# Kernel tuning notes

Measured on AMD Instinct MI355X. Metric: run time of the kernel, lower is better.

Reference implementation:

```python
import jax, jax.numpy as jnp
import numpy as np

HEADS = 4
DIM_HEAD = 32


def setup_inputs() -> dict:
    key = jax.random.key(0)
    k1, k2, k3, k4 = jax.random.split(key, 4)
    dim = 256
    hidden = HEADS * DIM_HEAD  # 128
    x = jax.random.normal(k1, (4, dim, 64, 64), dtype=jnp.float32)
    # 1x1 convs are channel-mixing matmuls; store weights as [out_ch, in_ch]
    w_qkv = jax.random.normal(k2, (3 * hidden, dim), dtype=jnp.float32) * (dim ** -0.5)
    w_out = jax.random.normal(k3, (dim, hidden), dtype=jnp.float32) * (hidden ** -0.5)
    b_out = jax.random.normal(k4, (dim,), dtype=jnp.float32) * 0.02
    return {"x": x, "w_qkv": w_qkv, "w_out": w_out, "b_out": b_out}


def reference(x, w_qkv, w_out, b_out):
    b, c, h, w = x.shape
    n = h * w
    scale = DIM_HEAD ** -0.5
    xf = x.reshape(b, c, n)                                   # b c n
    qkv = jnp.einsum('oc,bcn->bon', w_qkv, xf)                # b (3*H*D) n
    q, k, v = jnp.split(qkv, 3, axis=1)                       # each b (H*D) n
    q = q.reshape(b, HEADS, DIM_HEAD, n) * scale              # b h d n
    k = k.reshape(b, HEADS, DIM_HEAD, n)
    v = v.reshape(b, HEADS, DIM_HEAD, n)
    sim = jnp.einsum('bhdi,bhdj->bhij', q, k)                 # b h n n
    attn = jax.nn.softmax(sim, axis=-1)                       # stable max-subtract inside
    out = jnp.einsum('bhij,bhdj->bhdi', attn, v)              # b h d n
    out = out.reshape(b, HEADS * DIM_HEAD, n)                 # b (h d) n
    out = jnp.einsum('oc,bcn->bon', w_out, out) + b_out[None, :, None]
    return out.reshape(b, -1, h, w)
```

## Files before the change

### kernel.cpp

```cpp
#include <hip/hip_runtime.h>
#include <hip/hip_bf16.h>
#include <stdint.h>

#define B_SZ 4
#define C_IN 256
#define N_SP 4096
#define HEADS 4
#define DH 32
#define HID 128

#define BI 128
#define BJ 64
#define JHALF 2048
#define PP 68

typedef short short4v __attribute__((ext_vector_type(4)));
typedef short short8 __attribute__((ext_vector_type(8)));
typedef float f32x4 __attribute__((ext_vector_type(4)));

#if __has_builtin(__builtin_amdgcn_exp2f)
#define EXP2 __builtin_amdgcn_exp2f
#else
#define EXP2 exp2f
#endif

__device__ __forceinline__ short f2bfs(float f) {
  return (short)((__float_as_uint(f) + 0x8000u) >> 16);
}
__device__ __forceinline__ float bfs2f(short s) {
  return __uint_as_float(((uint32_t)(unsigned short)s) << 16);
}
__device__ __forceinline__ short8 ld_frag(const short* p) {
  short4v a = *(const short4v*)p;
  short4v b = *(const short4v*)(p + 4);
  return __builtin_shufflevector(a, b, 0, 1, 2, 3, 4, 5, 6, 7);
}
__device__ __forceinline__ f32x4 mfma16(short8 a, short8 b, f32x4 c) {
  return __builtin_amdgcn_mfma_f32_16x16x32_bf16(a, b, c, 0, 0, 0);
}

__global__ __launch_bounds__(256) void prep_k(
    const float* __restrict__ x, const float* __restrict__ w_qkv,
    const float* __restrict__ w_out,
    short* __restrict__ xh, short* __restrict__ xl,
    short* __restrict__ wqh, short* __restrict__ wql,
    short* __restrict__ woh, short* __restrict__ wol) {
  const int t = threadIdx.x;
  const int bx = blockIdx.x;
  if (bx < 1024) {
    __shared__ float T[64 * 65];
    const int b = bx >> 8, n0 = ((bx >> 2) & 63) * 64, c0 = (bx & 3) * 64;
    const float* xb = x + (size_t)b * C_IN * N_SP;
    {
      const int n = t & 63, cw = t >> 6;
#pragma unroll
      for (int i = 0; i < 16; ++i) {
        const int c = cw * 16 + i;
        T[n * 65 + c] = xb[(size_t)(c0 + c) * N_SP + n0 + n];
      }
    }
    __syncthreads();
    {
      const int n = t >> 2, cg = t & 3;
#pragma unroll
      for (int j = 0; j < 2; ++j) {
        const int c = cg * 16 + j * 8;
        short8 hv, lv;
#pragma unroll
        for (int e = 0; e < 8; ++e) {
          const float v = T[n * 65 + c + e];
          const short hh = f2bfs(v);
          hv[e] = hh;
          lv[e] = f2bfs(v - bfs2f(hh));
        }
        const size_t off = ((size_t)(b * N_SP + n0 + n)) * C_IN + c0 + c;
        *(short8*)(xh + off) = hv;
        *(short8*)(xl + off) = lv;
      }
    }
  } else {
    const int f0 = (bx - 1024) * 8192;
#pragma unroll
    for (int j = 0; j < 32; ++j) {
      const int f = f0 + j * 256 + t;
      float v;
      short *dh, *dl;
      int idx;
      if (f < 384 * 256) { v = w_qkv[f]; dh = wqh; dl = wql; idx = f; }
      else { idx = f - 384 * 256; v = w_out[idx]; dh = woh; dl = wol; }
      const short hh = f2bfs(v);
      dh[idx] = hh;
      dl[idx] = f2bfs(v - bfs2f(hh));
    }
  }
}

__global__ __launch_bounds__(256) void qkv_mfma_k(
    const short* __restrict__ xh, const short* __restrict__ xl,
    const short* __restrict__ wqh, const short* __restrict__ wql,
    short* __restrict__ qt, short* __restrict__ kt, short* __restrict__ vt) {
  const int t = threadIdx.x;
  const int lane = t & 63, w = t >> 6;
  const int l15 = lane & 15, quad = lane >> 4;
  const int osec = blockIdx.y, b = blockIdx.z;
  const int n0 = blockIdx.x * 64 + w * 16;
  const size_t xrow = ((size_t)(b * N_SP + n0 + l15)) * C_IN;
  const size_t wrow = ((size_t)(osec * 128 + l15)) * C_IN;
  const bool isv = (osec == 2);
  const f32x4 zz = {0.f, 0.f, 0.f, 0.f};
  f32x4 acc[8];
#pragma unroll
  for (int ot = 0; ot < 8; ++ot) acc[ot] = zz;

  for (int k0 = 0; k0 < C_IN; k0 += 32) {
    const int ko = k0 + quad * 8;
    const short8 xhf = *(const short8*)(xh + xrow + ko);
    const short8 xlf = *(const short8*)(xl + xrow + ko);
#pragma unroll
    for (int ot = 0; ot < 8; ++ot) {
      const size_t wo = wrow + (size_t)ot * 16 * C_IN + ko;
      const short8 whf = *(const short8*)(wqh + wo);
      const short8 wlf = *(const short8*)(wql + wo);
      if (isv) {
        acc[ot] = mfma16(xhf, whf, acc[ot]);
        acc[ot] = mfma16(xlf, whf, acc[ot]);
        acc[ot] = mfma16(xhf, wlf, acc[ot]);
      } else {
        acc[ot] = mfma16(whf, xhf, acc[ot]);
        acc[ot] = mfma16(whf, xlf, acc[ot]);
        acc[ot] = mfma16(wlf, xhf, acc[ot]);
      }
    }
  }

  if (!isv) {
    const float sc = osec ? 1.f : (0.17677669529663687f * 1.4426950408889634f);
    short* dst = osec ? kt : qt;
    const int n = n0 + l15;
#pragma unroll
    for (int ot = 0; ot < 8; ++ot) {
      const int ol = ot * 16 + quad * 4;
      const int h = ol >> 5, d0 = ol & 31;
      short4v p;
#pragma unroll
      for (int r = 0; r < 4; ++r) p[r] = f2bfs(acc[ot][r] * sc);
      *(short4v*)(dst + ((size_t)(b * HEADS + h) * N_SP + n) * DH + d0) = p;
    }
  } else {
    const int n = n0 + quad * 4;
#pragma unroll
    for (int ot = 0; ot < 8; ++ot) {
      const int ol = ot * 16 + l15;
      const int h = ol >> 5, d = ol & 31;
      short4v p;
#pragma unroll
      for (int r = 0; r < 4; ++r) p[r] = f2bfs(acc[ot][r]);
      *(short4v*)(vt + ((size_t)(b * HEADS + h) * DH + d) * N_SP + n) = p;
    }
  }
}

__global__ __launch_bounds__(256, 2) void attn_k(
    const short* __restrict__ qt, const short* __restrict__ kt,
    const short* __restrict__ vt, float* __restrict__ po,
    float* __restrict__ lws) {
  __shared__ short Ps[BI * PP];
  __shared__ float Osh[DH * 132];
  const int t = threadIdx.x;
  const int lane = t & 63, w = t >> 6;
  const int l15 = lane & 15, quad = lane >> 4;
  const int i0 = blockIdx.x * BI;
  const int bh = blockIdx.y;
  const int part = blockIdx.z;
  const int jbase = part * JHALF;
  const short* qg = qt + ((size_t)bh * N_SP + i0) * DH;
  const short* kg = kt + ((size_t)bh * N_SP + jbase) * DH;
  const short* vg = vt + (size_t)bh * DH * N_SP + jbase;

  short8 bq[2];
#pragma unroll
  for (int tt = 0; tt < 2; ++tt)
    bq[tt] = *(const short8*)(qg + (size_t)(w * 32 + tt * 16 + l15) * DH + quad * 8);

  const f32x4 zz = {0.f, 0.f, 0.f, 0.f};
  f32x4 o_acc[2][2] = {{zz, zz}, {zz, zz}};
  float lsum[2] = {0.f, 0.f};
  short* prow[2];
#pragma unroll
  for (int tt = 0; tt < 2; ++tt) prow[tt] = Ps + (w * 32 + tt * 16 + l15) * PP;

  short8 akA[4], akB[4], vbA[2][2], vbB[2][2];
#pragma unroll
  for (int jt = 0; jt < 4; ++jt)
    akA[jt] = *(const short8*)(kg + (size_t)(jt * 16 + l15) * DH + quad * 8);
#pragma unroll
  for (int dt = 0; dt < 2; ++dt)
#pragma unroll
    for (int kk = 0; kk < 2; ++kk)
      vbA[dt][kk] = *(const short8*)(vg + (size_t)(dt * 16 + l15) * N_SP + kk * 32 + quad * 8);

  auto body = [&](const short8 (&akc)[4], const short8 (&vbc)[2][2],
                  short8 (&akn)[4], short8 (&vbn)[2][2], int jn) {
    f32x4 sf[2][4];
    __builtin_amdgcn_s_setprio(1);
#pragma unroll
    for (int tt = 0; tt < 2; ++tt)
#pragma unroll
      for (int jt = 0; jt < 4; ++jt) sf[tt][jt] = mfma16(akc[jt], bq[tt], zz);
    __builtin_amdgcn_s_setprio(0);
#pragma unroll
    for (int jt = 0; jt < 4; ++jt)
      akn[jt] = *(const short8*)(kg + (size_t)(jn + jt * 16 + l15) * DH + quad * 8);
#pragma unroll
    for (int dt = 0; dt < 2; ++dt)
#pragma unroll
      for (int kk = 0; kk < 2; ++kk)
        vbn[dt][kk] = *(const short8*)(vg + (size_t)(dt * 16 + l15) * N_SP + jn + kk * 32 + quad * 8);
#pragma unroll
    for (int tt = 0; tt < 2; ++tt)
#pragma unroll
      for (int jt = 0; jt < 4; ++jt) {
        const float e0 = EXP2(sf[tt][jt][0]);
        const float e1 = EXP2(sf[tt][jt][1]);
        const float e2 = EXP2(sf[tt][jt][2]);
        const float e3 = EXP2(sf[tt][jt][3]);
        lsum[tt] += (e0 + e1) + (e2 + e3);
        uint2 pk;
        asm("v_cvt_pk_bf16_f32 %0, %1, %2" : "=v"(pk.x) : "v"(e0), "v"(e1));
        asm("v_cvt_pk_bf16_f32 %0, %1, %2" : "=v"(pk.y) : "v"(e2), "v"(e3));
        *(uint2*)(prow[tt] + jt * 16 + quad * 4) = pk;
      }
    asm volatile("s_waitcnt lgkmcnt(0)" ::: "memory");
    short8 pa[2][2];
#pragma unroll
    for (int tt = 0; tt < 2; ++tt)
#pragma unroll
      for (int kk = 0; kk < 2; ++kk) pa[tt][kk] = ld_frag(prow[tt] + kk * 32 + quad * 8);
    __builtin_amdgcn_s_setprio(1);
#pragma unroll
    for (int tt = 0; tt < 2; ++tt)
#pragma unroll
      for (int dt = 0; dt < 2; ++dt) {
        o_acc[tt][dt] = mfma16(pa[tt][0], vbc[dt][0], o_acc[tt][dt]);
        o_acc[tt][dt] = mfma16(pa[tt][1], vbc[dt][1], o_acc[tt][dt]);
      }
    __builtin_amdgcn_s_setprio(0);
  };

  for (int jo = 0; jo < JHALF; jo += 2 * BJ) {
    body(akA, vbA, akB, vbB, (jo + BJ) & (JHALF - 1));
    body(akB, vbB, akA, vbA, (jo + 2 * BJ) & (JHALF - 1));
  }

#pragma unroll
  for (int tt = 0; tt < 2; ++tt) {
    lsum[tt] += __shfl_xor(lsum[tt], 16);
    lsum[tt] += __shfl_xor(lsum[tt], 32);
  }
  if (lane < 16) {
#pragma unroll
    for (int tt = 0; tt < 2; ++tt)
      lws[((size_t)(part * 16 + bh)) * N_SP + i0 + w * 32 + tt * 16 + lane] = lsum[tt];
  }
#pragma unroll
  for (int tt = 0; tt < 2; ++tt)
#pragma unroll
    for (int dt = 0; dt < 2; ++dt)
#pragma unroll
      for (int r = 0; r < 4; ++r)
        Osh[(dt * 16 + l15) * 132 + w * 32 + tt * 16 + quad * 4 + r] = o_acc[tt][dt][r];
  __syncthreads();
  {
    const int ii = t & 127, half = t >> 7;
    const int b = bh >> 2, h = bh & 3;
    float* dst = po + ((size_t)((part * B_SZ + b) * N_SP) + i0 + ii) * HID +
                 h * 32 + half * 16;
#pragma unroll
    for (int j4 = 0; j4 < 4; ++j4) {
      float4 vv;
      vv.x = Osh[(half * 16 + j4 * 4 + 0) * 132 + ii];
      vv.y = Osh[(half * 16 + j4 * 4 + 1) * 132 + ii];
      vv.z = Osh[(half * 16 + j4 * 4 + 2) * 132 + ii];
      vv.w = Osh[(half * 16 + j4 * 4 + 3) * 132 + ii];
      *(float4*)(dst + j4 * 4) = vv;
    }
  }
}

__global__ __launch_bounds__(256) void out_mfma_k(
    const float* __restrict__ po, const float* __restrict__ lws,
    const short* __restrict__ woh, const short* __restrict__ wol,
    const float* __restrict__ bias, float* __restrict__ out) {
  const int t = threadIdx.x;
  const int lane = t & 63, w = t >> 6;
  const int l15 = lane & 15, quad = lane >> 4;
  const int osec = blockIdx.y, b = blockIdx.z;
  const int n0 = blockIdx.x * 64 + w * 16;
  const int n = n0 + l15;
  const size_t PSTR = (size_t)B_SZ * N_SP * HID;
  const float* arow = po + ((size_t)(b * N_SP) + n) * HID;
  const size_t wrow = ((size_t)(osec * 128 + l15)) * HID;
  const f32x4 zz = {0.f, 0.f, 0.f, 0.f};
  f32x4 acc[8];
#pragma unroll
  for (int ot = 0; ot < 8; ++ot) acc[ot] = zz;

  for (int k0 = 0; k0 < HID; k0 += 32) {
    const int ko = k0 + quad * 8;
    const int h = k0 >> 5;
    const int bh = b * HEADS + h;
    const float lv = lws[(size_t)bh * N_SP + n] + lws[(size_t)(16 + bh) * N_SP + n];
    const float linv = 1.f / lv;
    const float* pr = arow + ko;
    const float4 u0 = *(const float4*)(pr);
    const float4 u1 = *(const float4*)(pr + 4);
    const float4 v0 = *(const float4*)(pr + PSTR);
    const float4 v1 = *(const float4*)(pr + PSTR + 4);
    const float av[8] = {(u0.x + v0.x) * linv, (u0.y + v0.y) * linv,
                         (u0.z + v0.z) * linv, (u0.w + v0.w) * linv,
                         (u1.x + v1.x) * linv, (u1.y + v1.y) * linv,
                         (u1.z + v1.z) * linv, (u1.w + v1.w) * linv};
    short8 ahf, alf;
#pragma unroll
    for (int e = 0; e < 8; ++e) {
      const short hh = f2bfs(av[e]);
      ahf[e] = hh;
      alf[e] = f2bfs(av[e] - bfs2f(hh));
    }
#pragma unroll
    for (int ot = 0; ot < 8; ++ot) {
      const size_t wo = wrow + (size_t)ot * 16 * HID + ko;
      const short8 whf = *(const short8*)(woh + wo);
      const short8 wlf = *(const short8*)(wol + wo);
      acc[ot] = mfma16(ahf, whf, acc[ot]);
      acc[ot] = mfma16(alf, whf, acc[ot]);
      acc[ot] = mfma16(ahf, wlf, acc[ot]);
    }
  }
#pragma unroll
  for (int ot = 0; ot < 8; ++ot) {
    const int o = osec * 128 + ot * 16 + l15;
    const float bv = bias[o];
    float4 v = make_float4(acc[ot][0] + bv, acc[ot][1] + bv,
                           acc[ot][2] + bv, acc[ot][3] + bv);
    *(float4*)(out + ((size_t)(b * C_IN + o)) * N_SP + n0 + quad * 4) = v;
  }
}

extern "C" void kernel_launch(void* const* d_in, const int* in_sizes, int n_in,
                              void* d_out, int out_size, void* d_ws, size_t ws_size,
                              hipStream_t stream) {
  const float* x = (const float*)d_in[0];
  const float* w_qkv = (const float*)d_in[1];
  const float* w_out = (const float*)d_in[2];
  const float* b_out = (const float*)d_in[3];
  float* out = (float*)d_out;

  short* xh = (short*)d_ws;
  short* xl = xh + (size_t)B_SZ * N_SP * C_IN;
  short* wqh = xl + (size_t)B_SZ * N_SP * C_IN;
  short* wql = wqh + 384 * C_IN;
  short* woh = wql + 384 * C_IN;
  short* wol = woh + C_IN * HID;
  short* qt = wol + C_IN * HID;
  short* kt = qt + (size_t)16 * N_SP * DH;
  short* vt = kt + (size_t)16 * N_SP * DH;
  float* lws = (float*)(vt + (size_t)16 * N_SP * DH);
  float* po = (float*)xh;

  prep_k<<<dim3(1040), 256, 0, stream>>>(x, w_qkv, w_out, xh, xl, wqh, wql, woh, wol);
  qkv_mfma_k<<<dim3(64, 3, B_SZ), 256, 0, stream>>>(xh, xl, wqh, wql, qt, kt, vt);
  attn_k<<<dim3(N_SP / BI, B_SZ * HEADS, 2), 256, 0, stream>>>(qt, kt, vt, po, lws);
  out_mfma_k<<<dim3(64, 2, B_SZ), 256, 0, stream>>>(po, lws, woh, wol, b_out, out);
}
```

Before: 253.2 us.

## Compute softmax row sums via MFMA with ones vector, drop LDS epilogue

Replaces the per-element VALU accumulation of exp values with extra MFMA ops multiplying the bf16 probability tile by a vector of ones, so the row sums come out of the matrix unit. The sum now uses the bf16-rounded probabilities, which matches what the PV product uses. The shared-memory transpose and barrier in the epilogue are removed, and O is written straight from the accumulators with strided scalar global stores. The s_setprio hints around the MFMA blocks are also removed. The tradeoff is four extra MFMAs per iteration and less coalesced output stores.

```diff
diff --git a/kernel.cpp b/kernel.cpp
--- a/kernel.cpp
+++ b/kernel.cpp
@@ -165,7 +165,6 @@
     const short* __restrict__ vt, float* __restrict__ po,
     float* __restrict__ lws) {
   __shared__ short Ps[BI * PP];
-  __shared__ float Osh[DH * 132];
   const int t = threadIdx.x;
   const int lane = t & 63, w = t >> 6;
   const int l15 = lane & 15, quad = lane >> 4;
@@ -184,7 +183,10 @@
 
   const f32x4 zz = {0.f, 0.f, 0.f, 0.f};
   f32x4 o_acc[2][2] = {{zz, zz}, {zz, zz}};
-  float lsum[2] = {0.f, 0.f};
+  f32x4 l_acc[2] = {zz, zz};
+  short8 ones;
+#pragma unroll
+  for (int e = 0; e < 8; ++e) ones[e] = (short)0x3F80;
   short* prow[2];
 #pragma unroll
   for (int tt = 0; tt < 2; ++tt) prow[tt] = Ps + (w * 32 + tt * 16 + l15) * PP;
@@ -202,12 +204,10 @@
   auto body = [&](const short8 (&akc)[4], const short8 (&vbc)[2][2],
                   short8 (&akn)[4], short8 (&vbn)[2][2], int jn) {
     f32x4 sf[2][4];
-    __builtin_amdgcn_s_setprio(1);
 #pragma unroll
     for (int tt = 0; tt < 2; ++tt)
 #pragma unroll
       for (int jt = 0; jt < 4; ++jt) sf[tt][jt] = mfma16(akc[jt], bq[tt], zz);
-    __builtin_amdgcn_s_setprio(0);
 #pragma unroll
     for (int jt = 0; jt < 4; ++jt)
       akn[jt] = *(const short8*)(kg + (size_t)(jn + jt * 16 + l15) * DH + quad * 8);
@@ -224,7 +224,6 @@
         const float e1 = EXP2(sf[tt][jt][1]);
         const float e2 = EXP2(sf[tt][jt][2]);
         const float e3 = EXP2(sf[tt][jt][3]);
-        lsum[tt] += (e0 + e1) + (e2 + e3);
         uint2 pk;
         asm("v_cvt_pk_bf16_f32 %0, %1, %2" : "=v"(pk.x) : "v"(e0), "v"(e1));
         asm("v_cvt_pk_bf16_f32 %0, %1, %2" : "=v"(pk.y) : "v"(e2), "v"(e3));
@@ -236,15 +235,16 @@
     for (int tt = 0; tt < 2; ++tt)
 #pragma unroll
       for (int kk = 0; kk < 2; ++kk) pa[tt][kk] = ld_frag(prow[tt] + kk * 32 + quad * 8);
-    __builtin_amdgcn_s_setprio(1);
-#pragma unroll
-    for (int tt = 0; tt < 2; ++tt)
+#pragma unroll
+    for (int tt = 0; tt < 2; ++tt) {
 #pragma unroll
       for (int dt = 0; dt < 2; ++dt) {
         o_acc[tt][dt] = mfma16(pa[tt][0], vbc[dt][0], o_acc[tt][dt]);
         o_acc[tt][dt] = mfma16(pa[tt][1], vbc[dt][1], o_acc[tt][dt]);
       }
-    __builtin_amdgcn_s_setprio(0);
+      l_acc[tt] = mfma16(pa[tt][0], ones, l_acc[tt]);
+      l_acc[tt] = mfma16(pa[tt][1], ones, l_acc[tt]);
+    }
   };
 
   for (int jo = 0; jo < JHALF; jo += 2 * BJ) {
@@ -252,38 +252,25 @@
     body(akB, vbB, akA, vbA, (jo + 2 * BJ) & (JHALF - 1));
   }
 
-#pragma unroll
-  for (int tt = 0; tt < 2; ++tt) {
-    lsum[tt] += __shfl_xor(lsum[tt], 16);
-    lsum[tt] += __shfl_xor(lsum[tt], 32);
-  }
-  if (lane < 16) {
-#pragma unroll
-    for (int tt = 0; tt < 2; ++tt)
-      lws[((size_t)(part * 16 + bh)) * N_SP + i0 + w * 32 + tt * 16 + lane] = lsum[tt];
-  }
-#pragma unroll
-  for (int tt = 0; tt < 2; ++tt)
-#pragma unroll
-    for (int dt = 0; dt < 2; ++dt)
+  if (l15 == 0) {
+#pragma unroll
+    for (int tt = 0; tt < 2; ++tt)
 #pragma unroll
       for (int r = 0; r < 4; ++r)
-        Osh[(dt * 16 + l15) * 132 + w * 32 + tt * 16 + quad * 4 + r] = o_acc[tt][dt][r];
-  __syncthreads();
+        lws[((size_t)(part * 16 + bh)) * N_SP + i0 + w * 32 + tt * 16 + quad * 4 + r] =
+            l_acc[tt][r];
+  }
   {
-    const int ii = t & 127, half = t >> 7;
     const int b = bh >> 2, h = bh & 3;
-    float* dst = po + ((size_t)((part * B_SZ + b) * N_SP) + i0 + ii) * HID +
-                 h * 32 + half * 16;
-#pragma unroll
-    for (int j4 = 0; j4 < 4; ++j4) {
-      float4 vv;
-      vv.x = Osh[(half * 16 + j4 * 4 + 0) * 132 + ii];
-      vv.y = Osh[(half * 16 + j4 * 4 + 1) * 132 + ii];
-      vv.z = Osh[(half * 16 + j4 * 4 + 2) * 132 + ii];
-      vv.w = Osh[(half * 16 + j4 * 4 + 3) * 132 + ii];
-      *(float4*)(dst + j4 * 4) = vv;
-    }
+    float* pob = po + ((size_t)((part * B_SZ + b) * N_SP) + i0) * HID + h * 32;
+#pragma unroll
+    for (int tt = 0; tt < 2; ++tt)
+#pragma unroll
+      for (int dt = 0; dt < 2; ++dt)
+#pragma unroll
+        for (int r = 0; r < 4; ++r)
+          pob[(size_t)(w * 32 + tt * 16 + quad * 4 + r) * HID + dt * 16 + l15] =
+              o_acc[tt][dt][r];
   }
 }
 
```

Result: no change. 248.7 us (-1.8%).
